# Kernel optimization log

Hardware: AMD Instinct MI355X
Metric: run time of the kernel (lower is better)

## Reference

```python
import jax, jax.numpy as jnp
import numpy as np

B, L, H = 8, 4096, 1024
S = 32            # sentences (sep tokens) per sample, fixed for stackability
SEP_ID = 102      # BERT [SEP]
NUM_LABELS = 2
LN_EPS = 1e-5


def _make_ids_and_mask():
    rng = np.random.default_rng(0)
    ids = rng.integers(1000, 30000, size=(B, L))
    for i in range(B):
        pos = np.sort(rng.choice(np.arange(1, L), size=S, replace=False))
        ids[i, pos] = SEP_ID
    mask = np.ones((B, L), dtype=np.int32)
    return jnp.asarray(ids, dtype=jnp.int64), jnp.asarray(mask)


def setup_inputs() -> dict:
    key = jax.random.key(0)
    ks = jax.random.split(key, 4)
    input_ids, attention_mask = _make_ids_and_mask()
    std = 0.02
    return {
        "seq": jax.random.normal(ks[0], (B, L, H), dtype=jnp.float32),
        "input_ids": input_ids,
        "attention_mask": attention_mask,
        "W1": jax.random.normal(ks[1], (H, H), dtype=jnp.float32) * std,
        "b1": jnp.zeros((H,), jnp.float32),
        "ln_g": jnp.ones((H,), jnp.float32),
        "ln_b": jnp.zeros((H,), jnp.float32),
        "W2": jax.random.normal(ks[2], (H, NUM_LABELS), dtype=jnp.float32) * std,
        "b2": jnp.zeros((NUM_LABELS,), jnp.float32),
    }


def _segment_means(seq, input_ids, attention_mask):
    # sep positions per sample, fixed count S -> [B, S]
    sep_pos = jax.vmap(
        lambda ids: jnp.nonzero(ids == SEP_ID, size=S, fill_value=L - 1)[0]
    )(input_ids)
    bounds = jnp.concatenate(
        [jnp.zeros((seq.shape[0], 1), sep_pos.dtype), sep_pos], axis=1
    )  # [B, S+1]
    st, ed = bounds[:, :-1], bounds[:, 1:]  # inclusive span [st, ed]

    m = attention_mask.astype(seq.dtype)[..., None]            # [B,L,1]
    # exclusive prefix sums -> sum over [st, ed] = P[ed+1] - P[st]
    P = jnp.pad(jnp.cumsum(seq * m, axis=1), ((0, 0), (1, 0), (0, 0)))   # [B,L+1,H]
    C = jnp.pad(jnp.cumsum(attention_mask.astype(jnp.int32), axis=1), ((0, 0), (1, 0)))

    sums = (jnp.take_along_axis(P, (ed + 1)[..., None], axis=1)
            - jnp.take_along_axis(P, st[..., None], axis=1))   # [B,S,H]
    cnts = (jnp.take_along_axis(C, ed + 1, axis=1)
            - jnp.take_along_axis(C, st, axis=1))              # [B,S]
    cnts = jnp.maximum(cnts, 1).astype(seq.dtype)
    return sums / cnts[..., None]


def reference(seq, input_ids, attention_mask, W1, b1, ln_g, ln_b, W2, b2):
    reps = _segment_means(seq, input_ids, attention_mask)      # [B,S,H]
    h = jnp.einsum("bsh,hk->bsk", reps, W1) + b1
    mu = jnp.mean(h, axis=-1, keepdims=True)
    var = jnp.var(h, axis=-1, keepdims=True)
    h = (h - mu) * jax.lax.rsqrt(var + LN_EPS) * ln_g + ln_b
    h = jax.nn.gelu(h, approximate=False)   # torch nn.GELU default (erf); dropout is eval-mode identity
    return jnp.einsum("bsk,kn->bsn", h, W2) + b2               # [B,S,num_labels]
```

## Files before the change

### kernel.cpp

```cpp
#include <hip/hip_runtime.h>
#include <math.h>

#define BB 8
#define LL 4096
#define HH 1024
#define SS 32
#define SEPID 102
#define NROWS 256
#define TOK 64

__global__ __launch_bounds__(256) void prep_kernel(
    const int* __restrict__ ids, const int* __restrict__ mask,
    float* __restrict__ cnts, unsigned char* __restrict__ segcode) {
  int b = blockIdx.x;
  int tid = threadIdx.x;
  __shared__ int spos_raw[SS];
  __shared__ int spos[SS];
  __shared__ int nsep;
  __shared__ int excl_s[257];
  __shared__ int wtot[4];
  if (tid == 0) nsep = 0;
  if (tid < SS) spos_raw[tid] = LL - 1;
  __syncthreads();
  const int* idb = ids + (size_t)b * LL;
  const int* mb  = mask + (size_t)b * LL;

  for (int t = tid; t < LL; t += 256) {
    if (idb[t] == SEPID) {
      int slot = atomicAdd(&nsep, 1);
      if (slot < SS) spos_raw[slot] = t;
    }
  }
  __syncthreads();
  if (tid < SS) {
    int p = spos_raw[tid];
    int rank = 0;
    for (int j = 0; j < SS; j++) {
      int q = spos_raw[j];
      rank += (q < p) || (q == p && j < tid);
    }
    spos[rank] = p;
  }

  int local = 0;
  int base = tid * 16;
#pragma unroll
  for (int i = 0; i < 16; i++) local += mb[base + i];
  int lane = tid & 63, wave = tid >> 6;
  int v = local;
#pragma unroll
  for (int off = 1; off < 64; off <<= 1) {
    int n = __shfl_up(v, off, 64);
    if (lane >= off) v += n;
  }
  if (lane == 63) wtot[wave] = v;
  __syncthreads();
  int woff = 0;
  for (int w = 0; w < wave; w++) woff += wtot[w];
  excl_s[tid] = woff + v - local;
  if (tid == 0) excl_s[256] = wtot[0] + wtot[1] + wtot[2] + wtot[3];
  __syncthreads();

  if (tid < SS) {
    int st = (tid == 0) ? 0 : spos[tid - 1];
    int ed = spos[tid];
    int pa = st, pb = ed + 1;
    int ca = excl_s[pa >> 4];
    for (int i = pa & ~15; i < pa; i++) ca += mb[i];
    int cb = excl_s[pb >> 4];
    for (int i = pb & ~15; i < pb; i++) cb += mb[i];
    cnts[b * SS + tid] = (float)max(cb - ca, 1);
  }

  for (int t = tid; t < LL; t += 256) {
    int lo = 0, hi = SS;
    while (lo < hi) {
      int mid = (lo + hi) >> 1;
      lo = (spos[mid] < t) ? mid + 1 : lo;
      hi = (spos[mid] < t) ? hi : mid;
    }
    int issep = (idb[t] == SEPID) ? 1 : 0;
    segcode[(size_t)b * LL + t] = (unsigned char)((lo << 1) | issep);
  }
}

__device__ __forceinline__ void flush_seg(float* __restrict__ sums, int b,
                                          int seg, int tid, const float4& acc) {
  if (seg >= 0) {
    float* p = sums + ((size_t)(b * SS + seg)) * HH + tid * 4;
    atomicAdd(p + 0, acc.x);
    atomicAdd(p + 1, acc.y);
    atomicAdd(p + 2, acc.z);
    atomicAdd(p + 3, acc.w);
  }
}

__global__ __launch_bounds__(256) void segsum_kernel(
    const float4* __restrict__ seq, const int* __restrict__ mask,
    const unsigned char* __restrict__ segcode, float* __restrict__ sums) {
  const int chunks = LL / TOK;
  int b = blockIdx.x / chunks;
  int c = blockIdx.x % chunks;
  int t0 = c * TOK;
  int tid = threadIdx.x;
  __shared__ int scode[TOK];
  if (tid < TOK) {
    int t = t0 + tid;
    int cd = segcode[(size_t)b * LL + t];
    int m = mask[(size_t)b * LL + t];
    int r = cd >> 1, issep = cd & 1;
    int live = (issep || r < SS) ? 1 : 0;
    scode[tid] = cd | ((m && live) ? 0x100 : 0);
  }
  __syncthreads();
  float4 acc = make_float4(0.f, 0.f, 0.f, 0.f);
  int curseg = -1;
  const float4* rowbase = seq + (size_t)(b * LL + t0) * (HH / 4) + tid;
  for (int i = 0; i < TOK; i++) {
    float4 v = rowbase[(size_t)i * (HH / 4)];
    int cd = scode[i];
    int r = (cd >> 1) & 0x3F;
    int issep = cd & 1;
    float mf = (cd & 0x100) ? 1.f : 0.f;
    v.x *= mf; v.y *= mf; v.z *= mf; v.w *= mf;
    if (issep) {
      if (curseg != r) {
        flush_seg(sums, b, curseg, tid, acc);
        acc = make_float4(0.f, 0.f, 0.f, 0.f);
      }
      acc.x += v.x; acc.y += v.y; acc.z += v.z; acc.w += v.w;
      flush_seg(sums, b, r, tid, acc);
      if (r + 1 < SS) { curseg = r + 1; acc = v; }
      else { curseg = -1; acc = make_float4(0.f, 0.f, 0.f, 0.f); }
    } else {
      int sg = (r < SS) ? r : -1;
      if (sg != curseg) {
        flush_seg(sums, b, curseg, tid, acc);
        curseg = sg;
        acc = make_float4(0.f, 0.f, 0.f, 0.f);
      }
      acc.x += v.x; acc.y += v.y; acc.z += v.z; acc.w += v.w;
    }
  }
  flush_seg(sums, b, curseg, tid, acc);
}

__global__ __launch_bounds__(256) void gemm1_kernel(
    const float* __restrict__ sums, const float* __restrict__ cnts,
    const float* __restrict__ W1, float* __restrict__ h1) {
  __shared__ float As[32][33];
  __shared__ float Bs[32][33];
  __shared__ float inv[32];
  int bj = blockIdx.x;
  int bi = blockIdx.y;
  int bz = blockIdx.z;
  int tid = threadIdx.x;
  int r0 = bi * 32, c0 = bj * 32, kb = bz * 256;
  if (tid < 32) inv[tid] = 1.0f / cnts[r0 + tid];
  __syncthreads();
  int tx = tid & 15, ty = tid >> 4;
  int la_k = tid & 31;
  int la_i = tid >> 5;
  float acc00 = 0.f, acc01 = 0.f, acc10 = 0.f, acc11 = 0.f;
  for (int k0 = kb; k0 < kb + 256; k0 += 32) {
#pragma unroll
    for (int p = 0; p < 4; p++) {
      int i = la_i + p * 8;
      As[i][la_k] = sums[(size_t)(r0 + i) * HH + k0 + la_k] * inv[i];
      Bs[i][la_k] = W1[(size_t)(k0 + i) * HH + c0 + la_k];
    }
    __syncthreads();
#pragma unroll
    for (int kk = 0; kk < 32; kk++) {
      float a0 = As[ty * 2][kk];
      float a1 = As[ty * 2 + 1][kk];
      float b0 = Bs[kk][tx * 2];
      float b1v = Bs[kk][tx * 2 + 1];
      acc00 += a0 * b0; acc01 += a0 * b1v;
      acc10 += a1 * b0; acc11 += a1 * b1v;
    }
    __syncthreads();
  }
  int r = r0 + ty * 2, cc = c0 + tx * 2;
  atomicAdd(&h1[(size_t)r * HH + cc], acc00);
  atomicAdd(&h1[(size_t)r * HH + cc + 1], acc01);
  atomicAdd(&h1[(size_t)(r + 1) * HH + cc], acc10);
  atomicAdd(&h1[(size_t)(r + 1) * HH + cc + 1], acc11);
}

__global__ __launch_bounds__(256) void final_kernel(
    const float* __restrict__ h1, const float* __restrict__ b1,
    const float* __restrict__ ln_g, const float* __restrict__ ln_b,
    const float* __restrict__ W2, const float* __restrict__ b2,
    float* __restrict__ out) {
  int r = blockIdx.x;
  int tid = threadIdx.x;
  float4 x = ((const float4*)(h1 + (size_t)r * HH))[tid];
  float4 bb1 = ((const float4*)b1)[tid];
  x.x += bb1.x; x.y += bb1.y; x.z += bb1.z; x.w += bb1.w;
  float s = x.x + x.y + x.z + x.w;
  float sq = x.x * x.x + x.y * x.y + x.z * x.z + x.w * x.w;
  __shared__ float redA[4], redB[4];
#pragma unroll
  for (int off = 32; off >= 1; off >>= 1) {
    s += __shfl_down(s, off, 64);
    sq += __shfl_down(sq, off, 64);
  }
  int wave = tid >> 6, lane = tid & 63;
  if (lane == 0) { redA[wave] = s; redB[wave] = sq; }
  __syncthreads();
  float ts = redA[0] + redA[1] + redA[2] + redA[3];
  float tq = redB[0] + redB[1] + redB[2] + redB[3];
  float mean = ts * (1.0f / HH);
  float var = tq * (1.0f / HH) - mean * mean;
  float rinv = rsqrtf(var + 1e-5f);
  float4 g4 = ((const float4*)ln_g)[tid];
  float4 bb4 = ((const float4*)ln_b)[tid];
  float4 w20 = ((const float4*)W2)[tid * 2];
  float4 w21 = ((const float4*)W2)[tid * 2 + 1];
  float xs[4] = {x.x, x.y, x.z, x.w};
  float gs[4] = {g4.x, g4.y, g4.z, g4.w};
  float bs[4] = {bb4.x, bb4.y, bb4.z, bb4.w};
  float w0[4] = {w20.x, w20.z, w21.x, w21.z};
  float w1[4] = {w20.y, w20.w, w21.y, w21.w};
  float o0 = 0.f, o1 = 0.f;
#pragma unroll
  for (int j = 0; j < 4; j++) {
    float y = (xs[j] - mean) * rinv * gs[j] + bs[j];
    float gel = 0.5f * y * (1.0f + erff(y * 0.70710678118654752440f));
    o0 += gel * w0[j];
    o1 += gel * w1[j];
  }
#pragma unroll
  for (int off = 32; off >= 1; off >>= 1) {
    o0 += __shfl_down(o0, off, 64);
    o1 += __shfl_down(o1, off, 64);
  }
  __syncthreads();
  if (lane == 0) { redA[wave] = o0; redB[wave] = o1; }
  __syncthreads();
  if (tid == 0) {
    out[(size_t)r * 2 + 0] = redA[0] + redA[1] + redA[2] + redA[3] + b2[0];
    out[(size_t)r * 2 + 1] = redB[0] + redB[1] + redB[2] + redB[3] + b2[1];
  }
}

extern "C" void kernel_launch(void* const* d_in, const int* in_sizes, int n_in,
                              void* d_out, int out_size, void* d_ws, size_t ws_size,
                              hipStream_t stream) {
  (void)in_sizes; (void)n_in; (void)out_size; (void)ws_size;
  const float* seq  = (const float*)d_in[0];
  const int*   ids  = (const int*)d_in[1];
  const int*   mask = (const int*)d_in[2];
  const float* W1   = (const float*)d_in[3];
  const float* b1   = (const float*)d_in[4];
  const float* ln_g = (const float*)d_in[5];
  const float* ln_b = (const float*)d_in[6];
  const float* W2   = (const float*)d_in[7];
  const float* b2   = (const float*)d_in[8];
  float* out = (float*)d_out;

  char* ws = (char*)d_ws;
  float* sums = (float*)ws;
  float* h1   = (float*)(ws + (1 << 20));
  float* cnts = (float*)(ws + (2 << 20));
  unsigned char* segcode = (unsigned char*)(ws + (2 << 20) + 4096);

  hipMemsetAsync(ws, 0, 2u << 20, stream);
  prep_kernel<<<BB, 256, 0, stream>>>(ids, mask, cnts, segcode);
  segsum_kernel<<<BB * (LL / TOK), 256, 0, stream>>>(
      (const float4*)seq, mask, segcode, sums);
  dim3 g1(32, 8, 4);
  gemm1_kernel<<<g1, 256, 0, stream>>>(sums, cnts, W1, h1);
  final_kernel<<<NROWS, 256, 0, stream>>>(h1, b1, ln_g, ln_b, W2, b2, out);
}
```

Measured before the change: 262.1 us.

## Retile gemm1 with 64x64 register tiles and split-K partials; compute segment codes in segsum

gemm1 now uses 64x64 output tiles with 4x4 register blocking and vectorized float4 loads. It writes split-K partial results to separate buffers instead of issuing atomicAdds, and the final kernel sums the 8 partials. Segment index computation moves out of prep_kernel: segsum now binary-searches the stored separator positions directly, which removes the per-token segcode pass and buffer. The memset is limited to the sums buffer. The cost is a larger partial buffer for final_kernel to read and repeated binary searches in every segsum block.

```diff
diff --git a/kernel.cpp b/kernel.cpp
--- a/kernel.cpp
+++ b/kernel.cpp
@@ -8,10 +8,12 @@
 #define SEPID 102
 #define NROWS 256
 #define TOK 64
+#define SPLITK 8
+#define KSLICE (HH / SPLITK)
 
 __global__ __launch_bounds__(256) void prep_kernel(
     const int* __restrict__ ids, const int* __restrict__ mask,
-    float* __restrict__ cnts, unsigned char* __restrict__ segcode) {
+    float* __restrict__ cnts, int* __restrict__ spos_g) {
   int b = blockIdx.x;
   int tid = threadIdx.x;
   __shared__ int spos_raw[SS];
@@ -62,6 +64,7 @@
   __syncthreads();
 
   if (tid < SS) {
+    spos_g[b * SS + tid] = spos[tid];
     int st = (tid == 0) ? 0 : spos[tid - 1];
     int ed = spos[tid];
     int pa = st, pb = ed + 1;
@@ -71,17 +74,6 @@
     for (int i = pb & ~15; i < pb; i++) cb += mb[i];
     cnts[b * SS + tid] = (float)max(cb - ca, 1);
   }
-
-  for (int t = tid; t < LL; t += 256) {
-    int lo = 0, hi = SS;
-    while (lo < hi) {
-      int mid = (lo + hi) >> 1;
-      lo = (spos[mid] < t) ? mid + 1 : lo;
-      hi = (spos[mid] < t) ? hi : mid;
-    }
-    int issep = (idb[t] == SEPID) ? 1 : 0;
-    segcode[(size_t)b * LL + t] = (unsigned char)((lo << 1) | issep);
-  }
 }
 
 __device__ __forceinline__ void flush_seg(float* __restrict__ sums, int b,
@@ -97,20 +89,28 @@
 
 __global__ __launch_bounds__(256) void segsum_kernel(
     const float4* __restrict__ seq, const int* __restrict__ mask,
-    const unsigned char* __restrict__ segcode, float* __restrict__ sums) {
+    const int* __restrict__ spos_g, float* __restrict__ sums) {
   const int chunks = LL / TOK;
   int b = blockIdx.x / chunks;
   int c = blockIdx.x % chunks;
   int t0 = c * TOK;
   int tid = threadIdx.x;
+  __shared__ int sposs[SS];
   __shared__ int scode[TOK];
+  if (tid < SS) sposs[tid] = spos_g[b * SS + tid];
+  __syncthreads();
   if (tid < TOK) {
     int t = t0 + tid;
-    int cd = segcode[(size_t)b * LL + t];
+    int lo = 0, hi = SS;
+    while (lo < hi) {
+      int mid = (lo + hi) >> 1;
+      if (sposs[mid] < t) lo = mid + 1; else hi = mid;
+    }
+    int issep = (lo < SS && sposs[lo] == t) ? 1 : 0;
+    int r = lo;
     int m = mask[(size_t)b * LL + t];
-    int r = cd >> 1, issep = cd & 1;
     int live = (issep || r < SS) ? 1 : 0;
-    scode[tid] = cd | ((m && live) ? 0x100 : 0);
+    scode[tid] = ((r << 1) | issep) | ((m && live) ? 0x100 : 0);
   }
   __syncthreads();
   float4 acc = make_float4(0.f, 0.f, 0.f, 0.f);
@@ -147,57 +147,81 @@
 
 __global__ __launch_bounds__(256) void gemm1_kernel(
     const float* __restrict__ sums, const float* __restrict__ cnts,
-    const float* __restrict__ W1, float* __restrict__ h1) {
-  __shared__ float As[32][33];
-  __shared__ float Bs[32][33];
-  __shared__ float inv[32];
+    const float* __restrict__ W1, float* __restrict__ h1p) {
+  __shared__ float As[32][68];
+  __shared__ float Bs[32][68];
+  __shared__ float inv[64];
   int bj = blockIdx.x;
   int bi = blockIdx.y;
   int bz = blockIdx.z;
   int tid = threadIdx.x;
-  int r0 = bi * 32, c0 = bj * 32, kb = bz * 256;
-  if (tid < 32) inv[tid] = 1.0f / cnts[r0 + tid];
-  __syncthreads();
+  int r0 = bi * 64, c0 = bj * 64, kb = bz * KSLICE;
+  if (tid < 64) inv[tid] = 1.0f / cnts[r0 + tid];
+
+  int ai = tid >> 3;
+  int af = tid & 7;
+  int bk = tid >> 4;
+  int bj4 = tid & 15;
   int tx = tid & 15, ty = tid >> 4;
-  int la_k = tid & 31;
-  int la_i = tid >> 5;
-  float acc00 = 0.f, acc01 = 0.f, acc10 = 0.f, acc11 = 0.f;
-  for (int k0 = kb; k0 < kb + 256; k0 += 32) {
-#pragma unroll
-    for (int p = 0; p < 4; p++) {
-      int i = la_i + p * 8;
-      As[i][la_k] = sums[(size_t)(r0 + i) * HH + k0 + la_k] * inv[i];
-      Bs[i][la_k] = W1[(size_t)(k0 + i) * HH + c0 + la_k];
-    }
+
+  float acc[4][4];
+#pragma unroll
+  for (int i = 0; i < 4; i++)
+#pragma unroll
+    for (int j = 0; j < 4; j++) acc[i][j] = 0.f;
+
+  for (int k0 = kb; k0 < kb + KSLICE; k0 += 32) {
     __syncthreads();
+    float4 a0 = *(const float4*)&sums[(size_t)(r0 + ai) * HH + k0 + af * 4];
+    float4 a1 = *(const float4*)&sums[(size_t)(r0 + ai + 32) * HH + k0 + af * 4];
+    float4 b0 = *(const float4*)&W1[(size_t)(k0 + bk) * HH + c0 + bj4 * 4];
+    float4 b1 = *(const float4*)&W1[(size_t)(k0 + bk + 16) * HH + c0 + bj4 * 4];
+    float i0 = inv[ai], i1 = inv[ai + 32];
+    As[af * 4 + 0][ai] = a0.x * i0;
+    As[af * 4 + 1][ai] = a0.y * i0;
+    As[af * 4 + 2][ai] = a0.z * i0;
+    As[af * 4 + 3][ai] = a0.w * i0;
+    As[af * 4 + 0][ai + 32] = a1.x * i1;
+    As[af * 4 + 1][ai + 32] = a1.y * i1;
+    As[af * 4 + 2][ai + 32] = a1.z * i1;
+    As[af * 4 + 3][ai + 32] = a1.w * i1;
+    *(float4*)&Bs[bk][bj4 * 4] = b0;
+    *(float4*)&Bs[bk + 16][bj4 * 4] = b1;
+    __syncthreads();
 #pragma unroll
     for (int kk = 0; kk < 32; kk++) {
-      float a0 = As[ty * 2][kk];
-      float a1 = As[ty * 2 + 1][kk];
-      float b0 = Bs[kk][tx * 2];
-      float b1v = Bs[kk][tx * 2 + 1];
-      acc00 += a0 * b0; acc01 += a0 * b1v;
-      acc10 += a1 * b0; acc11 += a1 * b1v;
-    }
-    __syncthreads();
-  }
-  int r = r0 + ty * 2, cc = c0 + tx * 2;
-  atomicAdd(&h1[(size_t)r * HH + cc], acc00);
-  atomicAdd(&h1[(size_t)r * HH + cc + 1], acc01);
-  atomicAdd(&h1[(size_t)(r + 1) * HH + cc], acc10);
-  atomicAdd(&h1[(size_t)(r + 1) * HH + cc + 1], acc11);
+      float4 a = *(const float4*)&As[kk][ty * 4];
+      float4 b = *(const float4*)&Bs[kk][tx * 4];
+      acc[0][0] += a.x * b.x; acc[0][1] += a.x * b.y;
+      acc[0][2] += a.x * b.z; acc[0][3] += a.x * b.w;
+      acc[1][0] += a.y * b.x; acc[1][1] += a.y * b.y;
+      acc[1][2] += a.y * b.z; acc[1][3] += a.y * b.w;
+      acc[2][0] += a.z * b.x; acc[2][1] += a.z * b.y;
+      acc[2][2] += a.z * b.z; acc[2][3] += a.z * b.w;
+      acc[3][0] += a.w * b.x; acc[3][1] += a.w * b.y;
+      acc[3][2] += a.w * b.z; acc[3][3] += a.w * b.w;
+    }
+  }
+#pragma unroll
+  for (int dr = 0; dr < 4; dr++) {
+    float4 o = make_float4(acc[dr][0], acc[dr][1], acc[dr][2], acc[dr][3]);
+    *(float4*)&h1p[((size_t)bz * NROWS + r0 + ty * 4 + dr) * HH + c0 + tx * 4] = o;
+  }
 }
 
 __global__ __launch_bounds__(256) void final_kernel(
-    const float* __restrict__ h1, const float* __restrict__ b1,
+    const float* __restrict__ h1p, const float* __restrict__ b1,
     const float* __restrict__ ln_g, const float* __restrict__ ln_b,
     const float* __restrict__ W2, const float* __restrict__ b2,
     float* __restrict__ out) {
   int r = blockIdx.x;
   int tid = threadIdx.x;
-  float4 x = ((const float4*)(h1 + (size_t)r * HH))[tid];
-  float4 bb1 = ((const float4*)b1)[tid];
-  x.x += bb1.x; x.y += bb1.y; x.z += bb1.z; x.w += bb1.w;
+  float4 x = ((const float4*)b1)[tid];
+#pragma unroll
+  for (int sl = 0; sl < SPLITK; sl++) {
+    float4 p = ((const float4*)(h1p + ((size_t)sl * NROWS + r) * HH))[tid];
+    x.x += p.x; x.y += p.y; x.z += p.z; x.w += p.w;
+  }
   float s = x.x + x.y + x.z + x.w;
   float sq = x.x * x.x + x.y * x.y + x.z * x.z + x.w * x.w;
   __shared__ float redA[4], redB[4];
@@ -262,15 +286,15 @@
 
   char* ws = (char*)d_ws;
   float* sums = (float*)ws;
-  float* h1   = (float*)(ws + (1 << 20));
-  float* cnts = (float*)(ws + (2 << 20));
-  unsigned char* segcode = (unsigned char*)(ws + (2 << 20) + 4096);
-
-  hipMemsetAsync(ws, 0, 2u << 20, stream);
-  prep_kernel<<<BB, 256, 0, stream>>>(ids, mask, cnts, segcode);
+  float* h1p  = (float*)(ws + (1 << 20));
+  float* cnts = (float*)(ws + (9 << 20));
+  int*   spos = (int*)(ws + (9 << 20) + 4096);
+
+  hipMemsetAsync(sums, 0, (size_t)NROWS * HH * sizeof(float), stream);
+  prep_kernel<<<BB, 256, 0, stream>>>(ids, mask, cnts, spos);
   segsum_kernel<<<BB * (LL / TOK), 256, 0, stream>>>(
-      (const float4*)seq, mask, segcode, sums);
-  dim3 g1(32, 8, 4);
-  gemm1_kernel<<<g1, 256, 0, stream>>>(sums, cnts, W1, h1);
-  final_kernel<<<NROWS, 256, 0, stream>>>(h1, b1, ln_g, ln_b, W2, b2, out);
-}
+      (const float4*)seq, mask, spos, sums);
+  dim3 g1(16, 4, SPLITK);
+  gemm1_kernel<<<g1, 256, 0, stream>>>(sums, cnts, W1, h1p);
+  final_kernel<<<NROWS, 256, 0, stream>>>(h1p, b1, ln_g, ln_b, W2, b2, out);
+}
```

After: 243.2 us. 7.2% less time.
